# Optimization experiments

Hardware: AMD Instinct MI355X
Metric: run time of the kernel (lower is better)

Reference implementation:

```python
import jax, jax.numpy as jnp
import numpy as np

DIM, H, MAX_K, RADIUS, KNN_K, ALPHA, LN_EPS = 128, 4, 32, 0.3, 8, 2, 1e-5
DH = DIM // H
SCALE = DH ** -0.5


def _layernorm(x, w, b):
    mu = jnp.mean(x, axis=-1, keepdims=True)
    var = jnp.mean((x - mu) ** 2, axis=-1, keepdims=True)
    return (x - mu) * jax.lax.rsqrt(var + LN_EPS) * w + b


def setup_inputs() -> dict:
    key = jax.random.key(0)
    ks = jax.random.split(key, 12)
    N, M = 50000, 2500
    init = lambda k, shape: (jax.random.normal(k, shape, jnp.float32) * 0.02)
    return {
        "xyz": jax.random.normal(ks[0], (N, 3), jnp.float32),
        "feats": jax.random.normal(ks[1], (N, DIM), jnp.float32),
        "Wq": init(ks[2], (DIM, DIM)),
        "Wk": init(ks[3], (DIM, DIM)),
        "Wv": init(ks[4], (DIM, DIM)),
        "Wo": init(ks[5], (DIM, DIM)),
        "bo": jnp.zeros((DIM,), jnp.float32),
        "n1w": jnp.ones((DIM,), jnp.float32),
        "n1b": jnp.zeros((DIM,), jnp.float32),
        "n2w": jnp.ones((DIM,), jnp.float32),
        "n2b": jnp.zeros((DIM,), jnp.float32),
        "W1": init(ks[6], (DIM, 4 * DIM)),
        "b1": jnp.zeros((4 * DIM,), jnp.float32),
        "W2": init(ks[7], (4 * DIM, DIM)),
        "b2": jnp.zeros((DIM,), jnp.float32),
        "Wp": init(ks[8], (DIM, DIM)),
        "bp": jnp.zeros((DIM,), jnp.float32),
        "idx_center": jax.random.randint(ks[9], (M,), 0, N),
    }


def reference(xyz, feats, Wq, Wk, Wv, Wo, bo, n1w, n1b, n2w, n2b, W1, b1, W2, b2, Wp, bp, idx_center):
    M = idx_center.shape[0]
    center_xyz = xyz[idx_center]          # (M,3)
    center_feat = feats[idx_center]       # (M,C)

    # euclidean distance matrix (M,N) via |a|^2+|b|^2-2ab, safe sqrt (0-grad at 0 like torch.cdist)
    d2 = (jnp.sum(center_xyz ** 2, -1)[:, None] + jnp.sum(xyz ** 2, -1)[None, :]
          - 2.0 * center_xyz @ xyz.T)
    d2 = jnp.maximum(d2, 0.0)
    pos = d2 > 0
    dist = jnp.where(pos, jnp.sqrt(jnp.where(pos, d2, 1.0)), 0.0)  # (M,N)

    # ball query: mask + top-max_k smallest distances
    nbr_mask = dist < RADIUS
    nbr_mask = nbr_mask.at[jnp.arange(M), idx_center].set(True)
    dist_masked = jnp.where(nbr_mask, dist, jnp.inf)
    neg_d, nbr_idx = jax.lax.top_k(-dist_masked, MAX_K)   # (M,K)
    nbr_dist = -neg_d
    mask_valid = jnp.isfinite(nbr_dist)                    # (M,K)

    # gather neighbor feats, zero where invalid
    nbr_feats = jnp.where(mask_valid[..., None], feats[nbr_idx], 0.0)  # (M,K,C)

    # masked local attention per center (tiny heads)
    q = (center_feat @ Wq).reshape(M, H, DH)                       # (M,H,D)
    k = (nbr_feats @ Wk).reshape(M, MAX_K, H, DH).transpose(0, 2, 1, 3)  # (M,H,K,D)
    v = (nbr_feats @ Wv).reshape(M, MAX_K, H, DH).transpose(0, 2, 1, 3)
    attn = jnp.einsum('mhd,mhkd->mhk', q * SCALE, k)
    attn = jnp.where(mask_valid[:, None, :], attn, -1e9)
    attn = jax.nn.softmax(attn, axis=-1)
    out = jnp.einsum('mhk,mhkd->mhd', attn, v)
    # faithful to torch: transpose(1,2) before flatten -> (M, D, H) layout
    out = jnp.swapaxes(out, 1, 2).reshape(M, DIM)
    upd = out @ Wo + bo

    cf = center_feat + _layernorm(upd, n1w, n1b)
    ffn = jax.nn.relu(cf @ W1 + b1) @ W2 + b2
    cf = cf + _layernorm(ffn, n2w, n2b)

    # KNN inverse-distance-weighted upsample back to all N points
    neg_v, knn_idx = jax.lax.top_k(-dist.T, KNN_K)   # (N,k)
    knn_dist = -neg_v
    w = 1.0 / (knn_dist + 1e-6) ** ALPHA
    w = w / jnp.sum(w, axis=-1, keepdims=True)
    out_feats = jnp.einsum('nk,nkc->nc', w, cf[knn_idx])  # (N,C)
    out_feats = out_feats + jax.nn.relu(out_feats @ Wp + bp)
    return feats + out_feats
```

## Files before the change

kernel.cpp:

```cpp
#include <hip/hip_runtime.h>
#include <hip/hip_bf16.h>
#include <stdint.h>

#define DIM    128
#define KMAX   32
#define LN_EPS 1e-5f
#define ATT_SCALE 0.17677669529663687f
#define CAND   2048
#define WTOT   214400
#define PB     32
#define NSTR2  72
#define KSTR   132

typedef unsigned long long u64;
static __device__ __forceinline__ float bf2f(__hip_bfloat16 x) { return __bfloat162float(x); }

static __device__ __forceinline__ float norm32(float x, float y, float z) {
    return __fadd_rn(__fadd_rn(__fmul_rn(x, x), __fmul_rn(y, y)), __fmul_rn(z, z));
}
static __device__ __forceinline__ float d2_32(float cx, float cy, float cz, float cw,
                                              float px, float py, float pz, float pw) {
    float dot = __fmaf_rn(cz, pz, __fmaf_rn(cy, py, __fmul_rn(cx, px)));
    return __fsub_rn(__fadd_rn(cw, pw), __fmul_rn(2.0f, dot));
}
static __device__ __forceinline__ float d2_to_dist(float d2) {
    d2 = fmaxf(d2, 0.0f);
    return (d2 > 0.0f) ? __fsqrt_rn(d2) : 0.0f;
}
static __device__ __forceinline__ float dist32(float cx, float cy, float cz, float cw,
                                               float px, float py, float pz, float pw) {
    return d2_to_dist(d2_32(cx, cy, cz, cw, px, py, pz, pw));
}

static __device__ __forceinline__ float ldf(const void* p, int f32, size_t i) {
    return f32 ? ((const float*)p)[i] : bf2f(((const __hip_bfloat16*)p)[i]);
}
static __device__ __forceinline__ int ldidx(const void* p, int i64, int m) {
    return i64 ? ((const int*)p)[2 * m] : ((const int*)p)[m];
}

struct Ptrs { const void* p[18]; int sz[18]; };

__global__ void probe_dtypes(Ptrs P, int* __restrict__ fl) {
    int j = threadIdx.x;
    if (j >= 18) return;
    const void* x = P.p[j];
    int sz = P.sz[j];
    int flag = 0;
    if (j == 17) {
        const int* ip = (const int*)x;
        int odd_zero = 1, even_nz = 0;
        for (int k = 0; k < 8 && 2 * k + 1 < sz * 2; ++k) {
            if (ip[2 * k + 1] != 0) odd_zero = 0;
            if (ip[2 * k] != 0) even_nz = 1;
        }
        flag = (odd_zero && even_nz) ? 1 : 0;
    } else {
        const __hip_bfloat16* hp = (const __hip_bfloat16*)x;
        int n = sz < 256 ? sz : 256;
        for (int i = 0; i < n; ++i) {
            float w = bf2f(hp[i]);
            if (w != w || fabsf(w) > 1000.0f) { flag = 1; break; }
        }
        if ((j == 7 || j == 9) && bf2f(hp[0]) == 0.0f) flag = 1;
    }
    fl[j] = flag;
}

__global__ __launch_bounds__(256) void conv_params(Ptrs P, const int* __restrict__ fl,
                                                   float* __restrict__ Wf) {
    int i = blockIdx.x * 256 + threadIdx.x;
    if (i >= WTOT) return;
    int j, off;
    if      (i < 16384)  { j = 2;  off = i; }
    else if (i < 32768)  { j = 3;  off = i - 16384; }
    else if (i < 49152)  { j = 4;  off = i - 32768; }
    else if (i < 65536)  { j = 5;  off = i - 49152; }
    else if (i < 131072) { j = 11; off = i - 65536; }
    else if (i < 196608) { j = 13; off = i - 131072; }
    else if (i < 212992) { j = 15; off = i - 196608; }
    else if (i < 213120) { j = 6;  off = i - 212992; }
    else if (i < 213248) { j = 7;  off = i - 213120; }
    else if (i < 213376) { j = 8;  off = i - 213248; }
    else if (i < 213504) { j = 9;  off = i - 213376; }
    else if (i < 213632) { j = 10; off = i - 213504; }
    else if (i < 214144) { j = 12; off = i - 213632; }
    else if (i < 214272) { j = 14; off = i - 214144; }
    else                 { j = 16; off = i - 214272; }
    Wf[i] = ldf(P.p[j], fl[j], off);
}

__global__ void prep_pts(const void* __restrict__ xyz, const int* __restrict__ fl,
                         float4* __restrict__ pnt4, int N) {
    int i = blockIdx.x * 256 + threadIdx.x;
    if (i < N) {
        int f = fl[0];
        float x = ldf(xyz, f, 3 * i + 0), y = ldf(xyz, f, 3 * i + 1), z = ldf(xyz, f, 3 * i + 2);
        pnt4[i] = make_float4(x, y, z, norm32(x, y, z));
    }
}

__global__ void prep_ctrs(const void* __restrict__ idxc, const int* __restrict__ fl,
                          const float4* __restrict__ pnt4, float4* __restrict__ cent4,
                          int M, int N) {
    int m = blockIdx.x * 256 + threadIdx.x;
    if (m < M) {
        int c = ldidx(idxc, fl[17], m);
        c = (c >= 0 && c < N) ? c : 0;
        cent4[m] = pnt4[c];
    }
}

__global__ __launch_bounds__(256) void ball_scan(
    const float4* __restrict__ pnt4,
    const float4* __restrict__ cent4,
    int N, int* __restrict__ nbr_g) {

    __shared__ u64 key[CAND];
    __shared__ int s_cnt, s_ni[KMAX];

    int m = blockIdx.x, tid = threadIdx.x;
    float4 cc4 = cent4[m];

    if (tid == 0) s_cnt = 0;
    if (tid < KMAX) s_ni[tid] = -1;
    __syncthreads();

    for (int i = tid; i < N; i += 256) {
        float4 p = pnt4[i];
        float d2 = d2_32(cc4.x, cc4.y, cc4.z, cc4.w, p.x, p.y, p.z, p.w);
        if (d2 < 0.0901f) {
            float dist = d2_to_dist(d2);
            if (dist < 0.3f) {
                int pos = atomicAdd(&s_cnt, 1);
                if (pos < CAND)
                    key[pos] = ((u64)__float_as_uint(dist) << 32) | (unsigned)i;
            }
        }
    }
    __syncthreads();
    int cnt = min(s_cnt, CAND);

    for (int i = tid; i < cnt; i += 256) {
        u64 ki = key[i];
        int r = 0;
        for (int j = 0; j < cnt; ++j) r += (key[j] < ki) ? 1 : 0;
        if (r < KMAX) s_ni[r] = (int)(unsigned)(ki & 0xFFFFFFFFULL);
    }
    __syncthreads();
    if (tid < KMAX) nbr_g[m * KMAX + tid] = s_ni[tid];
}

#define NFT2(cc, kk) R[(cc) * NSTR2 + (kk)]
#define SKV2(kk, col) R[(kk) * KSTR + (col)]

__global__ __launch_bounds__(256, 4) void attn_ffn(
    const int* __restrict__ nbr_g,
    const void* __restrict__ feats,
    const void* __restrict__ idxc,
    const int* __restrict__ fl,
    const float* __restrict__ Wf,
    float* __restrict__ cf_out, int N, int M) {

    const float* Wqf = Wf;
    const float* Wkf = Wf + 16384;
    const float* Wvf = Wf + 32768;
    const float* Wof = Wf + 49152;
    const float* W1f = Wf + 65536;
    const float* W2f = Wf + 131072;
    const float* Pf  = Wf + 212992;

    __shared__ __align__(16) float R[128 * NSTR2];
    __shared__ int   s_ni[2 * KMAX];
    __shared__ __align__(16) float s_cf[256], s_x[256];
    __shared__ float s_red[8];

    int tid = threadIdx.x;
    int lane = tid & 63, wv = tid >> 6;
    int center = tid >> 7, col = tid & 127;
    int m0 = blockIdx.x * 2;
    int f1 = fl[1], fi = fl[17];

    if (tid < 64) {
        int m2 = m0 + (tid >> 5);
        s_ni[tid] = (m2 < M) ? nbr_g[m2 * KMAX + (tid & 31)] : -1;
    }
    {
        int m2 = m0 + center; m2 = (m2 < M) ? m2 : (M - 1);
        int c = ldidx(idxc, fi, m2);
        c = (c >= 0 && c < N) ? c : 0;
        s_cf[tid] = ldf(feats, f1, (size_t)c * DIM + col);
    }
    __syncthreads();
    for (int t = tid; t < 64 * DIM; t += 256) {
        int kk2 = t >> 7, cc = t & 127;
        int idx = s_ni[kk2];
        float v = (idx >= 0 && idx < N) ? ldf(feats, f1, (size_t)idx * DIM + cc) : 0.0f;
        NFT2(cc, kk2) = v;
    }
    __syncthreads();

    int kq = tid >> 5, cq = tid & 31;
    int k0 = kq * 8, c0 = cq * 4;
    float ka[8][4], va[8][4];
#pragma unroll
    for (int j = 0; j < 8; ++j)
#pragma unroll
        for (int cc2 = 0; cc2 < 4; ++cc2) { ka[j][cc2] = 0.0f; va[j][cc2] = 0.0f; }

#pragma unroll 2
    for (int i = 0; i < DIM; ++i) {
        float4 n0  = *(const float4*)&NFT2(i, k0);
        float4 n1  = *(const float4*)&NFT2(i, k0 + 4);
        float4 wk  = *(const float4*)&Wkf[i * DIM + c0];
        float4 wv4 = *(const float4*)&Wvf[i * DIM + c0];
        float nn[8] = {n0.x, n0.y, n0.z, n0.w, n1.x, n1.y, n1.z, n1.w};
#pragma unroll
        for (int j = 0; j < 8; ++j) {
            float nj = nn[j];
            ka[j][0] = fmaf(nj, wk.x, ka[j][0]);
            ka[j][1] = fmaf(nj, wk.y, ka[j][1]);
            ka[j][2] = fmaf(nj, wk.z, ka[j][2]);
            ka[j][3] = fmaf(nj, wk.w, ka[j][3]);
            va[j][0] = fmaf(nj, wv4.x, va[j][0]);
            va[j][1] = fmaf(nj, wv4.y, va[j][1]);
            va[j][2] = fmaf(nj, wv4.z, va[j][2]);
            va[j][3] = fmaf(nj, wv4.w, va[j][3]);
        }
    }
    __syncthreads();

    float* s_q    = R + 8448;
    float* s_attn = R + 8704;
    float* s_ao   = R + 8960;

#pragma unroll
    for (int j = 0; j < 8; ++j)
        *(float4*)&SKV2(k0 + j, c0) = make_float4(ka[j][0], ka[j][1], ka[j][2], ka[j][3]);
    {
        float acc = 0.0f;
        const float* cfc = s_cf + center * 128;
#pragma unroll 4
        for (int i = 0; i < DIM; i += 4) {
            float4 a = *(const float4*)&cfc[i];
            acc = fmaf(a.x, Wqf[(i + 0) * DIM + col], acc);
            acc = fmaf(a.y, Wqf[(i + 1) * DIM + col], acc);
            acc = fmaf(a.z, Wqf[(i + 2) * DIM + col], acc);
            acc = fmaf(a.w, Wqf[(i + 3) * DIM + col], acc);
        }
        s_q[tid] = acc;
    }
    __syncthreads();

    {
        int h = (tid >> 5) & 3, kk = tid & 31;
        float s = 0.0f;
#pragma unroll
        for (int d = 0; d < 32; ++d)
            s = fmaf(s_q[center * 128 + h * 32 + d], SKV2(center * 32 + kk, h * 32 + d), s);
        s *= ATT_SCALE;
        if (s_ni[center * 32 + kk] < 0) s = -1e9f;
        float mx = s;
        for (int off = 16; off; off >>= 1) mx = fmaxf(mx, __shfl_xor(mx, off, 32));
        float e = expf(s - mx);
        float sm = e;
        for (int off = 16; off; off >>= 1) sm += __shfl_xor(sm, off, 32);
        sm = (sm > 0.0f) ? sm : 1.0f;
        s_attn[tid] = e / sm;
    }
    __syncthreads();
#pragma unroll
    for (int j = 0; j < 8; ++j)
        *(float4*)&SKV2(k0 + j, c0) = make_float4(va[j][0], va[j][1], va[j][2], va[j][3]);
    __syncthreads();

    {
        int h = (tid >> 5) & 3, d = tid & 31;
        float o = 0.0f;
#pragma unroll
        for (int kk = 0; kk < KMAX; ++kk)
            o = fmaf(s_attn[center * 128 + h * 32 + kk], SKV2(center * 32 + kk, h * 32 + d), o);
        s_ao[center * 128 + d * 4 + h] = o;
    }
    __syncthreads();

    float upd = Pf[0 + col];
    {
#pragma unroll 4
        for (int i = 0; i < DIM; i += 4) {
            float4 a = *(const float4*)&s_ao[center * 128 + i];
            upd = fmaf(a.x, Wof[(i + 0) * DIM + col], upd);
            upd = fmaf(a.y, Wof[(i + 1) * DIM + col], upd);
            upd = fmaf(a.z, Wof[(i + 2) * DIM + col], upd);
            upd = fmaf(a.w, Wof[(i + 3) * DIM + col], upd);
        }
        float sum = upd;
        for (int off = 32; off; off >>= 1) sum += __shfl_xor(sum, off, 64);
        if (lane == 0) s_red[wv] = sum;
    }
    __syncthreads();
    float mu = (s_red[center * 2] + s_red[center * 2 + 1]) * (1.0f / 128.0f);
    float xc = upd - mu;
    {
        float q2 = xc * xc;
        for (int off = 32; off; off >>= 1) q2 += __shfl_xor(q2, off, 64);
        if (lane == 0) s_red[4 + wv] = q2;
    }
    __syncthreads();
    float var = (s_red[4 + center * 2] + s_red[5 + center * 2]) * (1.0f / 128.0f);
    float cf1;
    {
        float rs = 1.0f / sqrtf(var + LN_EPS);
        float ln1 = fmaf(xc * rs, Pf[128 + col], Pf[256 + col]);
        cf1 = s_cf[tid] + ln1;
        s_x[tid] = cf1;
    }
    __syncthreads();

    float* s_h = R;
#pragma unroll
    for (int jj = 0; jj < 4; ++jj) {
        int j = col + 128 * jj;
        float a = Pf[640 + j];
#pragma unroll 4
        for (int i = 0; i < DIM; i += 4) {
            float4 v = *(const float4*)&s_x[center * 128 + i];
            a = fmaf(v.x, W1f[(i + 0) * 512 + j], a);
            a = fmaf(v.y, W1f[(i + 1) * 512 + j], a);
            a = fmaf(v.z, W1f[(i + 2) * 512 + j], a);
            a = fmaf(v.w, W1f[(i + 3) * 512 + j], a);
        }
        s_h[center * 512 + j] = fmaxf(a, 0.0f);
    }
    __syncthreads();

    float fa = Pf[1152 + col];
    {
        const float* hc = s_h + center * 512;
#pragma unroll 4
        for (int i = 0; i < 256; i += 4) {
            float4 v = *(const float4*)&hc[i];
            fa = fmaf(v.x, W2f[(i + 0) * DIM + col], fa);
            fa = fmaf(v.y, W2f[(i + 1) * DIM + col], fa);
            fa = fmaf(v.z, W2f[(i + 2) * DIM + col], fa);
            fa = fmaf(v.w, W2f[(i + 3) * DIM + col], fa);
        }
    }
    float fb = 0.0f;
    {
        const float* hc = s_h + center * 512;
#pragma unroll 4
        for (int i = 256; i < 512; i += 4) {
            float4 v = *(const float4*)&hc[i];
            fb = fmaf(v.x, W2f[(i + 0) * DIM + col], fb);
            fb = fmaf(v.y, W2f[(i + 1) * DIM + col], fb);
            fb = fmaf(v.z, W2f[(i + 2) * DIM + col], fb);
            fb = fmaf(v.w, W2f[(i + 3) * DIM + col], fb);
        }
    }
    float ffn = fa + fb;
    {
        float sum = ffn;
        for (int off = 32; off; off >>= 1) sum += __shfl_xor(sum, off, 64);
        if (lane == 0) s_red[wv] = sum;
    }
    __syncthreads();
    mu = (s_red[center * 2] + s_red[center * 2 + 1]) * (1.0f / 128.0f);
    xc = ffn - mu;
    {
        float q2 = xc * xc;
        for (int off = 32; off; off >>= 1) q2 += __shfl_xor(q2, off, 64);
        if (lane == 0) s_red[4 + wv] = q2;
    }
    __syncthreads();
    var = (s_red[4 + center * 2] + s_red[5 + center * 2]) * (1.0f / 128.0f);
    {
        float rs2 = 1.0f / sqrtf(var + LN_EPS);
        float ln2 = fmaf(xc * rs2, Pf[384 + col], Pf[512 + col]);
        int m2 = m0 + center;
        if (m2 < M) cf_out[(size_t)m2 * DIM + col] = cf1 + ln2;
    }
}

#define CSWAP(a, b) { if ((b) < (a)) { u64 t_ = (a); (a) = (b); (b) = t_; } }

__global__ __launch_bounds__(256) void knn_select(
    const float4* __restrict__ pnt4,
    const float4* __restrict__ cent4,
    const float* __restrict__ cf,
    float* __restrict__ upg,
    int N, int M) {

    __shared__ u64 s_buf[4][64];
    __shared__ u64 s_srt[4][8];
    __shared__ int s_cnt[4];

    int lane = threadIdx.x & 63;
    int wv   = threadIdx.x >> 6;
    int p = blockIdx.x * 4 + wv;
    bool own = (p < N);

    float4 pp = make_float4(0.f, 0.f, 0.f, 0.f);
    if (own) pp = pnt4[p];

    if (lane == 0) s_cnt[wv] = 0;
    __syncthreads();

    float vmn = 3.4e38f;
    for (int j = lane; j < M; j += 64) {
        float4 cc = cent4[j];
        float d2 = d2_32(cc.x, cc.y, cc.z, cc.w, pp.x, pp.y, pp.z, pp.w);
        vmn = fminf(vmn, d2);
    }
    float vv = vmn, T = 0.0f;
#pragma unroll
    for (int e = 0; e < 8; ++e) {
        float mv = vv;
        for (int off = 32; off; off >>= 1) mv = fminf(mv, __shfl_xor(mv, off, 64));
        T = mv;
        if (vv == mv) vv = 3.4e38f;
    }
    float Tuse = fmaxf(T, 0.0f) * 1.0000019073486328f;

    for (int j = lane; j < M; j += 64) {
        float4 cc = cent4[j];
        float d2 = d2_32(cc.x, cc.y, cc.z, cc.w, pp.x, pp.y, pp.z, pp.w);
        if (d2 <= Tuse) {
            float dist = d2_to_dist(d2);
            u64 key = ((u64)__float_as_uint(dist) << 32) | (unsigned)j;
            int pos = atomicAdd(&s_cnt[wv], 1);
            if (pos < 64) s_buf[wv][pos] = key;
        }
    }
    __syncthreads();
    int cnt = s_cnt[wv];

    int   ki[8];
    float w8[8];
    float wsum = 0.0f;

    if (cnt <= 64 && M >= 8) {
        u64 myk = (lane < cnt) ? s_buf[wv][lane] : ~0ULL;
        int r = 0;
        for (int i = 0; i < cnt; ++i) {
            u64 o = s_buf[wv][i];
            r += (o < myk) ? 1 : 0;
        }
        if (lane < cnt && r < 8) s_srt[wv][r] = myk;
#pragma unroll
        for (int e = 0; e < 8; ++e) {
            u64 gm = s_srt[wv][e];
            float d = __uint_as_float((unsigned)(gm >> 32));
            int ci = (int)(unsigned)(gm & 0xFFFFFFFFULL);
            ci = (ci >= 0 && ci < M) ? ci : 0;
            float t = __fadd_rn(d, 1e-6f);
            float w = 1.0f / __fmul_rn(t, t);
            wsum += w;
            ki[e] = ci;
            w8[e] = w;
        }
    } else {
        u64 f0 = ~0ULL, f1_ = ~0ULL, f2_ = ~0ULL, f3 = ~0ULL,
            f4 = ~0ULL, f5 = ~0ULL, f6 = ~0ULL, f7 = ~0ULL;
        for (int j = lane; j < M; j += 64) {
            float4 cc = cent4[j];
            float dist = dist32(cc.x, cc.y, cc.z, cc.w, pp.x, pp.y, pp.z, pp.w);
            u64 key = ((u64)__float_as_uint(dist) << 32) | (unsigned)j;
            if (key < f7) {
                f7 = key;
                CSWAP(f6, f7); CSWAP(f5, f6); CSWAP(f4, f5); CSWAP(f3, f4);
                CSWAP(f2_, f3); CSWAP(f1_, f2_); CSWAP(f0, f1_);
            }
        }
        int ptr2 = 0;
        u64 cur2 = f0;
        wsum = 0.0f;
#pragma unroll
        for (int e = 0; e < 8; ++e) {
            u64 v = cur2;
            for (int off = 32; off; off >>= 1) {
                u64 o = __shfl_down(v, off, 64);
                v = (o < v) ? o : v;
            }
            u64 gm = __shfl(v, 0, 64);
            float d = __uint_as_float((unsigned)(gm >> 32));
            int ci = (int)(unsigned)(gm & 0xFFFFFFFFULL);
            ci = (ci >= 0 && ci < M) ? ci : 0;
            float t = __fadd_rn(d, 1e-6f);
            float w = 1.0f / __fmul_rn(t, t);
            wsum += w;
            ki[e] = ci;
            w8[e] = w;
            if (cur2 == gm) {
                ptr2++;
                cur2 = (ptr2 == 1) ? f1_ : (ptr2 == 2) ? f2_ : (ptr2 == 3) ? f3 :
                       (ptr2 == 4) ? f4 : (ptr2 == 5) ? f5 : (ptr2 == 6) ? f6 :
                       (ptr2 == 7) ? f7 : ~0ULL;
            }
        }
    }

    float inv = 1.0f / wsum;
#pragma unroll
    for (int e = 0; e < 8; ++e) w8[e] *= inv;

    int c0 = lane, c1 = lane + 64;
    float up0 = 0.0f, up1 = 0.0f;
#pragma unroll
    for (int k = 0; k < 8; ++k) {
        const float* row = cf + (size_t)ki[k] * DIM;
        up0 = fmaf(w8[k], row[c0], up0);
        up1 = fmaf(w8[k], row[c1], up1);
    }

    if (own) {
        upg[(size_t)p * DIM + c0] = up0;
        upg[(size_t)p * DIM + c1] = up1;
    }
}

__global__ __launch_bounds__(256) void wp_out(
    const float* __restrict__ Wf,
    const void* __restrict__ feats,
    const int* __restrict__ fl,
    float* __restrict__ out,
    int N) {

    const float* Wpf = Wf + 196608;
    const float* bpf = Wf + 212992 + 1280;

    __shared__ __align__(16) float s_up[PB][132];

    int tid = threadIdx.x;
    int p0 = blockIdx.x * PB;

    for (int f = tid; f < PB * 32; f += 256) {
        int p = f >> 5, i4 = (f & 31) << 2;
        float4 v = make_float4(0.f, 0.f, 0.f, 0.f);
        if (p0 + p < N) v = *(const float4*)&out[(size_t)(p0 + p) * DIM + i4];
        *(float4*)&s_up[p][i4] = v;
    }
    __syncthreads();

    int cq = tid & 31, pq = tid >> 5;
    int c0 = cq << 2;
    int pA = pq << 2;

    float a00 = 0.f, a01 = 0.f, a02 = 0.f, a03 = 0.f;
    float a10 = 0.f, a11 = 0.f, a12 = 0.f, a13 = 0.f;
    float a20 = 0.f, a21 = 0.f, a22 = 0.f, a23 = 0.f;
    float a30 = 0.f, a31 = 0.f, a32 = 0.f, a33 = 0.f;

#pragma unroll 4
    for (int i = 0; i < DIM; ++i) {
        float4 w = *(const float4*)&Wpf[(size_t)i * DIM + c0];
        float u0 = s_up[pA + 0][i];
        float u1 = s_up[pA + 1][i];
        float u2 = s_up[pA + 2][i];
        float u3 = s_up[pA + 3][i];
        a00 = fmaf(u0, w.x, a00); a01 = fmaf(u0, w.y, a01);
        a02 = fmaf(u0, w.z, a02); a03 = fmaf(u0, w.w, a03);
        a10 = fmaf(u1, w.x, a10); a11 = fmaf(u1, w.y, a11);
        a12 = fmaf(u1, w.z, a12); a13 = fmaf(u1, w.w, a13);
        a20 = fmaf(u2, w.x, a20); a21 = fmaf(u2, w.y, a21);
        a22 = fmaf(u2, w.z, a22); a23 = fmaf(u2, w.w, a23);
        a30 = fmaf(u3, w.x, a30); a31 = fmaf(u3, w.y, a31);
        a32 = fmaf(u3, w.z, a32); a33 = fmaf(u3, w.w, a33);
    }

    int f1v = fl[1];
    float4 bp4 = make_float4(bpf[c0 + 0], bpf[c0 + 1], bpf[c0 + 2], bpf[c0 + 3]);

    float accs[4][4] = {{a00, a01, a02, a03}, {a10, a11, a12, a13},
                        {a20, a21, a22, a23}, {a30, a31, a32, a33}};
#pragma unroll
    for (int a = 0; a < 4; ++a) {
        int p = p0 + pA + a;
        if (p < N) {
            float4 u = *(const float4*)&s_up[pA + a][c0];
            float4 o;
            o.x = ldf(feats, f1v, (size_t)p * DIM + c0 + 0) + u.x + fmaxf(bp4.x + accs[a][0], 0.0f);
            o.y = ldf(feats, f1v, (size_t)p * DIM + c0 + 1) + u.y + fmaxf(bp4.y + accs[a][1], 0.0f);
            o.z = ldf(feats, f1v, (size_t)p * DIM + c0 + 2) + u.z + fmaxf(bp4.z + accs[a][2], 0.0f);
            o.w = ldf(feats, f1v, (size_t)p * DIM + c0 + 3) + u.w + fmaxf(bp4.w + accs[a][3], 0.0f);
            *(float4*)&out[(size_t)p * DIM + c0] = o;
        }
    }
}

extern "C" void kernel_launch(void* const* d_in, const int* in_sizes, int n_in,
                              void* d_out, int out_size, void* d_ws, size_t ws_size,
                              hipStream_t stream) {
    int N = in_sizes[0] / 3;
    int M = in_sizes[17];

    Ptrs P;
    for (int j = 0; j < 18; ++j) { P.p[j] = d_in[j]; P.sz[j] = in_sizes[j]; }

    size_t off = 0;
    auto alloc = [&](size_t bytes) -> void* {
        off = (off + 255) & ~(size_t)255;
        void* p = (void*)((char*)d_ws + off);
        off += bytes;
        return p;
    };
    int*    fl    = (int*)alloc(32 * 4);
    float*  Wf    = (float*)alloc((size_t)WTOT * 4);
    float4* pnt4  = (float4*)alloc((size_t)N * 16);
    float4* cent4 = (float4*)alloc((size_t)M * 16);
    float*  cfbuf = (float*)alloc((size_t)M * DIM * 4);
    int*    nbr   = (int*)alloc((size_t)M * KMAX * 4);

    probe_dtypes<<<1, 32, 0, stream>>>(P, fl);
    conv_params<<<(WTOT + 255) / 256, 256, 0, stream>>>(P, fl, Wf);
    prep_pts<<<(N + 255) / 256, 256, 0, stream>>>(d_in[0], fl, pnt4, N);
    prep_ctrs<<<(M + 255) / 256, 256, 0, stream>>>(d_in[17], fl, pnt4, cent4, M, N);
    ball_scan<<<M, 256, 0, stream>>>(pnt4, cent4, N, nbr);
    attn_ffn<<<(M + 1) / 2, 256, 0, stream>>>(nbr, d_in[1], d_in[17], fl, Wf, cfbuf, N, M);
    knn_select<<<(N + 3) / 4, 256, 0, stream>>>(pnt4, cent4, cfbuf, (float*)d_out, N, M);
    wp_out<<<(N + PB - 1) / PB, 256, 0, stream>>>(Wf, d_in[1], fl, (float*)d_out, N);
}
```

Before: 553.8 us.

## Process two points per wave in knn_select and fuse prep kernels

knn_select now has each wavefront handle two query points. Every center float4 loaded in the two scans over all centers is reused for two distance evaluations, and the two independent reductions give more ILP. Separately, the parameter conversion, point prep and center prep kernels are merged into one launch, and centers are recomputed from xyz directly so they no longer depend on pnt4. The cost is more registers per thread and half as many knn blocks, which could lower occupancy.

```diff
diff --git a/kernel.cpp b/kernel.cpp
--- a/kernel.cpp
+++ b/kernel.cpp
@@ -67,47 +67,49 @@
     fl[j] = flag;
 }
 
-__global__ __launch_bounds__(256) void conv_params(Ptrs P, const int* __restrict__ fl,
-                                                   float* __restrict__ Wf) {
-    int i = blockIdx.x * 256 + threadIdx.x;
-    if (i >= WTOT) return;
-    int j, off;
-    if      (i < 16384)  { j = 2;  off = i; }
-    else if (i < 32768)  { j = 3;  off = i - 16384; }
-    else if (i < 49152)  { j = 4;  off = i - 32768; }
-    else if (i < 65536)  { j = 5;  off = i - 49152; }
-    else if (i < 131072) { j = 11; off = i - 65536; }
-    else if (i < 196608) { j = 13; off = i - 131072; }
-    else if (i < 212992) { j = 15; off = i - 196608; }
-    else if (i < 213120) { j = 6;  off = i - 212992; }
-    else if (i < 213248) { j = 7;  off = i - 213120; }
-    else if (i < 213376) { j = 8;  off = i - 213248; }
-    else if (i < 213504) { j = 9;  off = i - 213376; }
-    else if (i < 213632) { j = 10; off = i - 213504; }
-    else if (i < 214144) { j = 12; off = i - 213632; }
-    else if (i < 214272) { j = 14; off = i - 214144; }
-    else                 { j = 16; off = i - 214272; }
-    Wf[i] = ldf(P.p[j], fl[j], off);
-}
-
-__global__ void prep_pts(const void* __restrict__ xyz, const int* __restrict__ fl,
-                         float4* __restrict__ pnt4, int N) {
-    int i = blockIdx.x * 256 + threadIdx.x;
-    if (i < N) {
-        int f = fl[0];
-        float x = ldf(xyz, f, 3 * i + 0), y = ldf(xyz, f, 3 * i + 1), z = ldf(xyz, f, 3 * i + 2);
-        pnt4[i] = make_float4(x, y, z, norm32(x, y, z));
-    }
-}
-
-__global__ void prep_ctrs(const void* __restrict__ idxc, const int* __restrict__ fl,
-                          const float4* __restrict__ pnt4, float4* __restrict__ cent4,
-                          int M, int N) {
-    int m = blockIdx.x * 256 + threadIdx.x;
-    if (m < M) {
-        int c = ldidx(idxc, fl[17], m);
-        c = (c >= 0 && c < N) ? c : 0;
-        cent4[m] = pnt4[c];
+__global__ __launch_bounds__(256) void conv_prep(Ptrs P, const int* __restrict__ fl,
+                                                 float* __restrict__ Wf,
+                                                 float4* __restrict__ pnt4,
+                                                 float4* __restrict__ cent4,
+                                                 int N, int M, int convB) {
+    int b = blockIdx.x;
+    if (b < convB) {
+        int i = b * 256 + threadIdx.x;
+        if (i >= WTOT) return;
+        int j, off;
+        if      (i < 16384)  { j = 2;  off = i; }
+        else if (i < 32768)  { j = 3;  off = i - 16384; }
+        else if (i < 49152)  { j = 4;  off = i - 32768; }
+        else if (i < 65536)  { j = 5;  off = i - 49152; }
+        else if (i < 131072) { j = 11; off = i - 65536; }
+        else if (i < 196608) { j = 13; off = i - 131072; }
+        else if (i < 212992) { j = 15; off = i - 196608; }
+        else if (i < 213120) { j = 6;  off = i - 212992; }
+        else if (i < 213248) { j = 7;  off = i - 213120; }
+        else if (i < 213376) { j = 8;  off = i - 213248; }
+        else if (i < 213504) { j = 9;  off = i - 213376; }
+        else if (i < 213632) { j = 10; off = i - 213504; }
+        else if (i < 214144) { j = 12; off = i - 213632; }
+        else if (i < 214272) { j = 14; off = i - 214144; }
+        else                 { j = 16; off = i - 214272; }
+        Wf[i] = ldf(P.p[j], fl[j], off);
+    } else {
+        int i = (b - convB) * 256 + threadIdx.x;
+        int f0 = fl[0];
+        if (i < N) {
+            float x = ldf(P.p[0], f0, 3 * i + 0);
+            float y = ldf(P.p[0], f0, 3 * i + 1);
+            float z = ldf(P.p[0], f0, 3 * i + 2);
+            pnt4[i] = make_float4(x, y, z, norm32(x, y, z));
+        }
+        if (i < M) {
+            int c = ldidx(P.p[17], fl[17], i);
+            c = (c >= 0 && c < N) ? c : 0;
+            float x = ldf(P.p[0], f0, 3 * c + 0);
+            float y = ldf(P.p[0], f0, 3 * c + 1);
+            float z = ldf(P.p[0], f0, 3 * c + 2);
+            cent4[i] = make_float4(x, y, z, norm32(x, y, z));
+        }
     }
 }
 
@@ -384,6 +386,18 @@
 
 #define CSWAP(a, b) { if ((b) < (a)) { u64 t_ = (a); (a) = (b); (b) = t_; } }
 
+static __device__ __forceinline__ float extract8(float vmn) {
+    float vv = vmn, T = 0.0f;
+#pragma unroll
+    for (int e = 0; e < 8; ++e) {
+        float mv = vv;
+        for (int off = 32; off; off >>= 1) mv = fminf(mv, __shfl_xor(mv, off, 64));
+        T = mv;
+        if (vv == mv) vv = 3.4e38f;
+    }
+    return fmaxf(T, 0.0f) * 1.0000019073486328f;
+}
+
 __global__ __launch_bounds__(256) void knn_select(
     const float4* __restrict__ pnt4,
     const float4* __restrict__ cent4,
@@ -391,131 +405,141 @@
     float* __restrict__ upg,
     int N, int M) {
 
-    __shared__ u64 s_buf[4][64];
-    __shared__ u64 s_srt[4][8];
-    __shared__ int s_cnt[4];
-
-    int lane = threadIdx.x & 63;
-    int wv   = threadIdx.x >> 6;
-    int p = blockIdx.x * 4 + wv;
-    bool own = (p < N);
-
-    float4 pp = make_float4(0.f, 0.f, 0.f, 0.f);
-    if (own) pp = pnt4[p];
-
-    if (lane == 0) s_cnt[wv] = 0;
-    __syncthreads();
-
-    float vmn = 3.4e38f;
+    __shared__ u64 s_buf[4][2][64];
+    __shared__ u64 s_srt[4][2][8];
+    __shared__ int s_cnt[4][2];
+
+    int tid = threadIdx.x;
+    int lane = tid & 63, wv = tid >> 6;
+    int p0 = blockIdx.x * 8 + wv * 2;
+    bool ownA = (p0 < N), ownB = (p0 + 1 < N);
+
+    float4 pa = make_float4(0.f, 0.f, 0.f, 0.f);
+    float4 pb = make_float4(0.f, 0.f, 0.f, 0.f);
+    if (ownA) pa = pnt4[p0];
+    if (ownB) pb = pnt4[p0 + 1];
+
+    if (lane < 2) s_cnt[wv][lane] = 0;
+    __syncthreads();
+
+    float va = 3.4e38f, vb = 3.4e38f;
     for (int j = lane; j < M; j += 64) {
         float4 cc = cent4[j];
-        float d2 = d2_32(cc.x, cc.y, cc.z, cc.w, pp.x, pp.y, pp.z, pp.w);
-        vmn = fminf(vmn, d2);
-    }
-    float vv = vmn, T = 0.0f;
-#pragma unroll
-    for (int e = 0; e < 8; ++e) {
-        float mv = vv;
-        for (int off = 32; off; off >>= 1) mv = fminf(mv, __shfl_xor(mv, off, 64));
-        T = mv;
-        if (vv == mv) vv = 3.4e38f;
-    }
-    float Tuse = fmaxf(T, 0.0f) * 1.0000019073486328f;
+        va = fminf(va, d2_32(cc.x, cc.y, cc.z, cc.w, pa.x, pa.y, pa.z, pa.w));
+        vb = fminf(vb, d2_32(cc.x, cc.y, cc.z, cc.w, pb.x, pb.y, pb.z, pb.w));
+    }
+    float Ta = extract8(va);
+    float Tb = extract8(vb);
 
     for (int j = lane; j < M; j += 64) {
         float4 cc = cent4[j];
-        float d2 = d2_32(cc.x, cc.y, cc.z, cc.w, pp.x, pp.y, pp.z, pp.w);
-        if (d2 <= Tuse) {
-            float dist = d2_to_dist(d2);
+        float d2a = d2_32(cc.x, cc.y, cc.z, cc.w, pa.x, pa.y, pa.z, pa.w);
+        float d2b = d2_32(cc.x, cc.y, cc.z, cc.w, pb.x, pb.y, pb.z, pb.w);
+        if (d2a <= Ta) {
+            float dist = d2_to_dist(d2a);
             u64 key = ((u64)__float_as_uint(dist) << 32) | (unsigned)j;
-            int pos = atomicAdd(&s_cnt[wv], 1);
-            if (pos < 64) s_buf[wv][pos] = key;
-        }
-    }
-    __syncthreads();
-    int cnt = s_cnt[wv];
-
-    int   ki[8];
-    float w8[8];
-    float wsum = 0.0f;
-
-    if (cnt <= 64 && M >= 8) {
-        u64 myk = (lane < cnt) ? s_buf[wv][lane] : ~0ULL;
-        int r = 0;
-        for (int i = 0; i < cnt; ++i) {
-            u64 o = s_buf[wv][i];
-            r += (o < myk) ? 1 : 0;
-        }
-        if (lane < cnt && r < 8) s_srt[wv][r] = myk;
-#pragma unroll
-        for (int e = 0; e < 8; ++e) {
-            u64 gm = s_srt[wv][e];
+            int pos = atomicAdd(&s_cnt[wv][0], 1);
+            if (pos < 64) s_buf[wv][0][pos] = key;
+        }
+        if (d2b <= Tb) {
+            float dist = d2_to_dist(d2b);
+            u64 key = ((u64)__float_as_uint(dist) << 32) | (unsigned)j;
+            int pos = atomicAdd(&s_cnt[wv][1], 1);
+            if (pos < 64) s_buf[wv][1][pos] = key;
+        }
+    }
+
+    int   ki[2][8];
+    float w8[2][8];
+    float wsum[2];
+
+#pragma unroll
+    for (int e = 0; e < 2; ++e) {
+        int cnt = s_cnt[wv][e];
+        if (cnt <= 64 && M >= 8) {
+            u64 myk = (lane < cnt) ? s_buf[wv][e][lane] : ~0ULL;
+            int r = 0;
+            for (int i = 0; i < cnt; ++i) {
+                u64 o = s_buf[wv][e][i];
+                r += (o < myk) ? 1 : 0;
+            }
+            if (lane < cnt && r < 8) s_srt[wv][e][r] = myk;
+        } else {
+            float4 pp = e ? pb : pa;
+            u64 f0 = ~0ULL, f1_ = ~0ULL, f2_ = ~0ULL, f3 = ~0ULL,
+                f4 = ~0ULL, f5 = ~0ULL, f6 = ~0ULL, f7 = ~0ULL;
+            for (int j = lane; j < M; j += 64) {
+                float4 cc = cent4[j];
+                float dist = dist32(cc.x, cc.y, cc.z, cc.w, pp.x, pp.y, pp.z, pp.w);
+                u64 key = ((u64)__float_as_uint(dist) << 32) | (unsigned)j;
+                if (key < f7) {
+                    f7 = key;
+                    CSWAP(f6, f7); CSWAP(f5, f6); CSWAP(f4, f5); CSWAP(f3, f4);
+                    CSWAP(f2_, f3); CSWAP(f1_, f2_); CSWAP(f0, f1_);
+                }
+            }
+            int ptr2 = 0;
+            u64 cur2 = f0;
+#pragma unroll
+            for (int e2 = 0; e2 < 8; ++e2) {
+                u64 v = cur2;
+                for (int off = 32; off; off >>= 1) {
+                    u64 o = __shfl_down(v, off, 64);
+                    v = (o < v) ? o : v;
+                }
+                u64 gm = __shfl(v, 0, 64);
+                if (lane == 0) s_srt[wv][e][e2] = gm;
+                if (cur2 == gm) {
+                    ptr2++;
+                    cur2 = (ptr2 == 1) ? f1_ : (ptr2 == 2) ? f2_ : (ptr2 == 3) ? f3 :
+                           (ptr2 == 4) ? f4 : (ptr2 == 5) ? f5 : (ptr2 == 6) ? f6 :
+                           (ptr2 == 7) ? f7 : ~0ULL;
+                }
+            }
+        }
+        float ws = 0.0f;
+#pragma unroll
+        for (int e2 = 0; e2 < 8; ++e2) {
+            u64 gm = s_srt[wv][e][e2];
             float d = __uint_as_float((unsigned)(gm >> 32));
             int ci = (int)(unsigned)(gm & 0xFFFFFFFFULL);
             ci = (ci >= 0 && ci < M) ? ci : 0;
             float t = __fadd_rn(d, 1e-6f);
             float w = 1.0f / __fmul_rn(t, t);
-            wsum += w;
-            ki[e] = ci;
-            w8[e] = w;
-        }
-    } else {
-        u64 f0 = ~0ULL, f1_ = ~0ULL, f2_ = ~0ULL, f3 = ~0ULL,
-            f4 = ~0ULL, f5 = ~0ULL, f6 = ~0ULL, f7 = ~0ULL;
-        for (int j = lane; j < M; j += 64) {
-            float4 cc = cent4[j];
-            float dist = dist32(cc.x, cc.y, cc.z, cc.w, pp.x, pp.y, pp.z, pp.w);
-            u64 key = ((u64)__float_as_uint(dist) << 32) | (unsigned)j;
-            if (key < f7) {
-                f7 = key;
-                CSWAP(f6, f7); CSWAP(f5, f6); CSWAP(f4, f5); CSWAP(f3, f4);
-                CSWAP(f2_, f3); CSWAP(f1_, f2_); CSWAP(f0, f1_);
-            }
-        }
-        int ptr2 = 0;
-        u64 cur2 = f0;
-        wsum = 0.0f;
-#pragma unroll
-        for (int e = 0; e < 8; ++e) {
-            u64 v = cur2;
-            for (int off = 32; off; off >>= 1) {
-                u64 o = __shfl_down(v, off, 64);
-                v = (o < v) ? o : v;
-            }
-            u64 gm = __shfl(v, 0, 64);
-            float d = __uint_as_float((unsigned)(gm >> 32));
-            int ci = (int)(unsigned)(gm & 0xFFFFFFFFULL);
-            ci = (ci >= 0 && ci < M) ? ci : 0;
-            float t = __fadd_rn(d, 1e-6f);
-            float w = 1.0f / __fmul_rn(t, t);
-            wsum += w;
-            ki[e] = ci;
-            w8[e] = w;
-            if (cur2 == gm) {
-                ptr2++;
-                cur2 = (ptr2 == 1) ? f1_ : (ptr2 == 2) ? f2_ : (ptr2 == 3) ? f3 :
-                       (ptr2 == 4) ? f4 : (ptr2 == 5) ? f5 : (ptr2 == 6) ? f6 :
-                       (ptr2 == 7) ? f7 : ~0ULL;
-            }
-        }
-    }
-
-    float inv = 1.0f / wsum;
-#pragma unroll
-    for (int e = 0; e < 8; ++e) w8[e] *= inv;
+            ws += w;
+            ki[e][e2] = ci;
+            w8[e][e2] = w;
+        }
+        wsum[e] = ws;
+    }
+
+    float invA = 1.0f / wsum[0];
+    float invB = 1.0f / wsum[1];
+#pragma unroll
+    for (int k = 0; k < 8; ++k) { w8[0][k] *= invA; w8[1][k] *= invB; }
 
     int c0 = lane, c1 = lane + 64;
-    float up0 = 0.0f, up1 = 0.0f;
+    float uA0 = 0.0f, uA1 = 0.0f, uB0 = 0.0f, uB1 = 0.0f;
 #pragma unroll
     for (int k = 0; k < 8; ++k) {
-        const float* row = cf + (size_t)ki[k] * DIM;
-        up0 = fmaf(w8[k], row[c0], up0);
-        up1 = fmaf(w8[k], row[c1], up1);
-    }
-
-    if (own) {
-        upg[(size_t)p * DIM + c0] = up0;
-        upg[(size_t)p * DIM + c1] = up1;
+        const float* row = cf + (size_t)ki[0][k] * DIM;
+        uA0 = fmaf(w8[0][k], row[c0], uA0);
+        uA1 = fmaf(w8[0][k], row[c1], uA1);
+    }
+#pragma unroll
+    for (int k = 0; k < 8; ++k) {
+        const float* row = cf + (size_t)ki[1][k] * DIM;
+        uB0 = fmaf(w8[1][k], row[c0], uB0);
+        uB1 = fmaf(w8[1][k], row[c1], uB1);
+    }
+
+    if (ownA) {
+        upg[(size_t)p0 * DIM + c0] = uA0;
+        upg[(size_t)p0 * DIM + c1] = uA1;
+    }
+    if (ownB) {
+        upg[(size_t)(p0 + 1) * DIM + c0] = uB0;
+        upg[(size_t)(p0 + 1) * DIM + c1] = uB1;
     }
 }
 
@@ -611,12 +635,14 @@
     float*  cfbuf = (float*)alloc((size_t)M * DIM * 4);
     int*    nbr   = (int*)alloc((size_t)M * KMAX * 4);
 
+    int convB = (WTOT + 255) / 256;
+    int NM = (N > M) ? N : M;
+    int prepB = (NM + 255) / 256;
+
     probe_dtypes<<<1, 32, 0, stream>>>(P, fl);
-    conv_params<<<(WTOT + 255) / 256, 256, 0, stream>>>(P, fl, Wf);
-    prep_pts<<<(N + 255) / 256, 256, 0, stream>>>(d_in[0], fl, pnt4, N);
-    prep_ctrs<<<(M + 255) / 256, 256, 0, stream>>>(d_in[17], fl, pnt4, cent4, M, N);
+    conv_prep<<<convB + prepB, 256, 0, stream>>>(P, fl, Wf, pnt4, cent4, N, M, convB);
     ball_scan<<<M, 256, 0, stream>>>(pnt4, cent4, N, nbr);
     attn_ffn<<<(M + 1) / 2, 256, 0, stream>>>(nbr, d_in[1], d_in[17], fl, Wf, cfbuf, N, M);
-    knn_select<<<(N + 3) / 4, 256, 0, stream>>>(pnt4, cent4, cfbuf, (float*)d_out, N, M);
+    knn_select<<<(N + 7) / 8, 256, 0, stream>>>(pnt4, cent4, cfbuf, (float*)d_out, N, M);
     wp_out<<<(N + PB - 1) / PB, 256, 0, stream>>>(Wf, d_in[1], fl, (float*)d_out, N);
 }
```

New measurement: 511.7 us. 7.6% less time.
